# Kernel tuning notes

Measured on AMD Instinct MI355X. Metric: run time of the kernel, lower is better.

Reference implementation:

```python
import jax, jax.numpy as jnp
import numpy as np

B, N, E, ED, H, HID, OUT = 128, 100, 3200, 8, 4, 16, 32


def _ln(x, g, b):
    m = x.mean(-1, keepdims=True)
    v = ((x - m) ** 2).mean(-1, keepdims=True)
    return (x - m) / jnp.sqrt(v + 1e-5) * g + b


def _seg_softmax(logits, seg, n):
    # logits: [Etot, H], seg: [Etot] target node ids
    m = jax.ops.segment_max(logits, seg, num_segments=n)
    ex = jnp.exp(logits - m[seg])
    s = jax.ops.segment_sum(ex, seg, num_segments=n)
    return ex / (s[seg] + 1e-16)


def _tconv(x, src, dst, ea, Wq, bq, Wk, bk, Wv, bv, We, Ws, bs, heads, ch, n):
    # PyG TransformerConv, concat=False, root_weight=True, beta=False
    q = (x @ Wq.T + bq).reshape(-1, heads, ch)
    k = (x @ Wk.T + bk).reshape(-1, heads, ch)
    v = (x @ Wv.T + bv).reshape(-1, heads, ch)
    e = (ea @ We.T).reshape(-1, heads, ch)
    alpha = (q[dst] * (k[src] + e)).sum(-1) / jnp.sqrt(jnp.float32(ch))  # [Etot,H]
    alpha = _seg_softmax(alpha, dst, n)
    msg = (v[src] + e) * alpha[..., None]
    out = jax.ops.segment_sum(msg, dst, num_segments=n)  # [n,H,ch]
    out = out.mean(axis=1)  # concat=False -> head mean
    return out + x @ Ws.T + bs


def setup_inputs() -> dict:
    key = jax.random.key(0)
    ks = jax.random.split(key, 32)
    d = {}
    d['nodes_feats'] = jax.random.randint(ks[0], (B, N, 1), 0, 5).astype(jnp.float32)
    d['edge_index'] = jax.random.randint(ks[1], (B, 2, E), 0, N).astype(jnp.int32)
    d['edge_attr'] = jax.random.normal(ks[2], (B, E, ED), jnp.float32)
    d['agent_id'] = jax.random.randint(ks[3], (B, 1), 0, N).astype(jnp.int32)
    s = 0.1
    d['entity_embed'] = jax.random.normal(ks[4], (5, 4), jnp.float32)
    d['W1'] = jax.random.normal(ks[5], (HID, 4 + ED), jnp.float32) * s
    d['b1'] = jnp.zeros((HID,), jnp.float32)
    d['W2'] = jax.random.normal(ks[6], (HID, HID), jnp.float32) * s
    d['b2'] = jnp.zeros((HID,), jnp.float32)
    d['W3'] = jax.random.normal(ks[7], (HID, HID), jnp.float32) * s
    d['b3'] = jnp.zeros((HID,), jnp.float32)
    d['ln_g'] = jnp.ones((HID,), jnp.float32)
    d['ln_b'] = jnp.zeros((HID,), jnp.float32)
    i = 8
    for pre, ch, outd in (('g1', HID, HID), ('g2', OUT, OUT)):
        d[pre + '_Wq'] = jax.random.normal(ks[i + 0], (H * ch, HID), jnp.float32) * s
        d[pre + '_bq'] = jnp.zeros((H * ch,), jnp.float32)
        d[pre + '_Wk'] = jax.random.normal(ks[i + 1], (H * ch, HID), jnp.float32) * s
        d[pre + '_bk'] = jnp.zeros((H * ch,), jnp.float32)
        d[pre + '_Wv'] = jax.random.normal(ks[i + 2], (H * ch, HID), jnp.float32) * s
        d[pre + '_bv'] = jnp.zeros((H * ch,), jnp.float32)
        d[pre + '_We'] = jax.random.normal(ks[i + 3], (H * ch, ED), jnp.float32) * s
        d[pre + '_Ws'] = jax.random.normal(ks[i + 4], (outd, HID), jnp.float32) * s
        d[pre + '_bs'] = jnp.zeros((outd,), jnp.float32)
        i += 5
    return d


def reference(nodes_feats, edge_index, edge_attr, agent_id, entity_embed,
              W1, b1, W2, b2, W3, b3, ln_g, ln_b,
              g1_Wq, g1_bq, g1_Wk, g1_bk, g1_Wv, g1_bv, g1_We, g1_Ws, g1_bs,
              g2_Wq, g2_bq, g2_Wk, g2_bk, g2_Wv, g2_bv, g2_We, g2_Ws, g2_bs):
    n_tot = B * N
    # batched graph -> flat graph with per-batch node offsets
    offs = (jnp.arange(B, dtype=edge_index.dtype) * N)[:, None, None]
    ei = (edge_index + offs).transpose(1, 0, 2).reshape(2, -1)  # [2, B*E]
    src, dst = ei[0], ei[1]
    x = nodes_feats.reshape(-1, 1)            # [n_tot, 1]
    ea = edge_attr.reshape(-1, ED)            # [B*E, ED]

    # Embedding message-passing layer (aggr='add')
    etype = x[:, 0].astype(jnp.int32)[src]
    emb = entity_embed[etype]                  # [Etot, 4]
    h = jnp.concatenate([emb, ea], axis=1)
    h = _ln(jax.nn.relu(h @ W1.T + b1), ln_g, ln_b)
    h = _ln(jax.nn.relu(h @ W2.T + b2), ln_g, ln_b)
    h = _ln(jax.nn.relu(h @ W3.T + b3), ln_g, ln_b)
    z = jax.ops.segment_sum(h, dst, num_segments=n_tot)  # [n_tot, 16]

    a = _tconv(z, src, dst, ea, g1_Wq, g1_bq, g1_Wk, g1_bk, g1_Wv, g1_bv,
               g1_We, g1_Ws, g1_bs, H, HID, n_tot)
    a = _tconv(a, src, dst, ea, g2_Wq, g2_bq, g2_Wk, g2_bk, g2_Wv, g2_bv,
               g2_We, g2_Ws, g2_bs, H, OUT, n_tot)
    a = jax.nn.relu(a).reshape(B, N, OUT)
    # graph_aggr == 'agent': gather the agent node per batch
    out = jnp.take_along_axis(a, agent_id[:, :, None].astype(jnp.int32), axis=1)
    return out[:, 0, :]  # [B, OUT]
```

## Files before the change

kernel.cpp:

```cpp
#include <hip/hip_runtime.h>
#include <math.h>
#include <stdint.h>

#define Bb   128
#define Nn   100
#define Ee   3200
#define NTOT (Bb*Nn)
#define ETOT (Bb*Ee)



__global__ __launch_bounds__(1024) void k_csr(const int* __restrict__ ei,
                                              const int* __restrict__ agent,
                                              int* __restrict__ off,
                                              int2* __restrict__ cpair,
                                              int* __restrict__ mark)
{
    int b = ((blockIdx.x & 7) << 4) + (blockIdx.x >> 3);
    int t = threadIdx.x;
    __shared__ int s_src[Ee];
    __shared__ int s_dst[Ee];
    __shared__ int cnt[128];
    __shared__ int exc[128];
    __shared__ int cur[128];
    if (t < 128) cnt[t] = 0;
    if (t < Nn) mark[b * Nn + t] = 0;
    __syncthreads();
    const int* eis = ei + (size_t)b * 2 * Ee;
    const int* eid = eis + Ee;
    for (int e = t; e < Ee; e += 1024) {
        int s = eis[e];
        int d = eid[e];
        s_src[e] = s;
        s_dst[e] = d;
        atomicAdd(&cnt[d], 1);
    }
    __syncthreads();
    if (t < 64) {
        int c0 = cnt[2 * t];
        int c1 = cnt[2 * t + 1];
        int p = c0 + c1;
#pragma unroll
        for (int d = 1; d < 64; d <<= 1) {
            int v = __shfl_up(p, d);
            if (t >= d) p += v;
        }
        exc[2 * t]     = p - c0 - c1;
        exc[2 * t + 1] = p - c1;
        cur[2 * t]     = p - c0 - c1;
        cur[2 * t + 1] = p - c1;
    }
    __syncthreads();
    if (t < Nn) off[b * Nn + t] = b * Ee + exc[t];
    if (b == Bb - 1 && t == 0) off[NTOT] = ETOT;
    for (int e = t; e < Ee; e += 1024) {
        int d = s_dst[e];
        int idx = atomicAdd(&cur[d], 1);
        cpair[b * Ee + idx] = make_int2(s_src[e] + b * Nn, b * Ee + e);
    }
    int an = agent[b];
    if (t == 0) mark[b * Nn + an] = 1;
    for (int e = t; e < Ee; e += 1024) {
        if (s_dst[e] == an) mark[b * Nn + s_src[e]] = 1;
    }
}


__device__ __forceinline__ void ln_reg(float* h, const float* __restrict__ g,
                                       const float* __restrict__ b) {
    float s = 0.f;
#pragma unroll
    for (int c = 0; c < 16; c++) s += h[c];
    float m = s * 0.0625f;
    float v = 0.f;
#pragma unroll
    for (int c = 0; c < 16; c++) { float d = h[c] - m; v += d * d; }
    float r = rsqrtf(v * 0.0625f + 1e-5f);
#pragma unroll
    for (int c = 0; c < 16; c++) h[c] = (h[c] - m) * r * g[c] + b[c];
}

__global__ __launch_bounds__(256) void k_mlpz(
    const float* __restrict__ nf, const float* __restrict__ ea, const float* __restrict__ ee,
    const float* __restrict__ W1, const float* __restrict__ b1,
    const float* __restrict__ W2, const float* __restrict__ b2,
    const float* __restrict__ W3, const float* __restrict__ b3,
    const float* __restrict__ lg, const float* __restrict__ lb,
    const float* __restrict__ Wk, const float* __restrict__ bk,
    const float* __restrict__ Wv, const float* __restrict__ bv,
    const int* __restrict__ off, const int2* __restrict__ cpair,
    float* __restrict__ z, float* __restrict__ k1, float* __restrict__ v1)
{
    int lane = threadIdx.x & 63;
    int wid  = threadIdx.x >> 6;
    int n    = (blockIdx.x & 7) * (NTOT / 8) + (blockIdx.x >> 3) * 4 + wid;

    int o0 = off[n];
    int deg = off[n + 1] - o0;
    int chunks = (deg + 63) >> 6;

    float zs[16];
#pragma unroll
    for (int c = 0; c < 16; c++) zs[c] = 0.f;

    for (int ch = 0; ch < chunks; ch++) {
        int i = ch * 64 + lane;
        float h3[16];
        if (i < deg) {
            int2 p = cpair[o0 + i];
            int et = (int)nf[p.x];
            float in[12];
#pragma unroll
            for (int j = 0; j < 4; j++) in[j] = ee[et * 4 + j];
            const float4* ea4 = (const float4*)(ea + (size_t)p.y * 8);
            float4 ua = ea4[0], ub = ea4[1];
            in[4] = ua.x; in[5] = ua.y; in[6] = ua.z; in[7] = ua.w;
            in[8] = ub.x; in[9] = ub.y; in[10] = ub.z; in[11] = ub.w;

            float h1[16];
#pragma unroll
            for (int c = 0; c < 16; c++) {
                float s = b1[c];
#pragma unroll
                for (int j = 0; j < 12; j++) s = fmaf(W1[c * 12 + j], in[j], s);
                h1[c] = fmaxf(s, 0.f);
            }
            ln_reg(h1, lg, lb);
            float h2[16];
#pragma unroll
            for (int c = 0; c < 16; c++) {
                float s = b2[c];
#pragma unroll
                for (int j = 0; j < 16; j++) s = fmaf(W2[c * 16 + j], h1[j], s);
                h2[c] = fmaxf(s, 0.f);
            }
            ln_reg(h2, lg, lb);
#pragma unroll
            for (int c = 0; c < 16; c++) {
                float s = b3[c];
#pragma unroll
                for (int j = 0; j < 16; j++) s = fmaf(W3[c * 16 + j], h2[j], s);
                h3[c] = fmaxf(s, 0.f);
            }
            ln_reg(h3, lg, lb);
        } else {
#pragma unroll
            for (int c = 0; c < 16; c++) h3[c] = 0.f;
        }
#pragma unroll
        for (int c = 0; c < 16; c++) {
            float s = h3[c];
            s += __shfl_xor(s, 1);
            s += __shfl_xor(s, 2);
            s += __shfl_xor(s, 4);
            s += __shfl_xor(s, 8);
            s += __shfl_xor(s, 16);
            s += __shfl_xor(s, 32);
            zs[c] += s;
        }
    }

#pragma unroll
    for (int c = 0; c < 16; c++) if (lane == c) z[n * 16 + c] = zs[c];

    float ak = bk[lane], av = bv[lane];
#pragma unroll
    for (int j = 0; j < 16; j++) {
        ak = fmaf(Wk[lane * 16 + j], zs[j], ak);
        av = fmaf(Wv[lane * 16 + j], zs[j], av);
    }
    k1[n * 64 + lane] = ak;
    v1[n * 64 + lane] = av;
}


__global__ __launch_bounds__(256) void k_attn1(
    const float* __restrict__ ea,
    const float* __restrict__ k1, const float* __restrict__ v1,
    const float* __restrict__ z, const int* __restrict__ mark,
    const float* __restrict__ Wq, const float* __restrict__ bq,
    const float* __restrict__ We, const float* __restrict__ Ws, const float* __restrict__ bs,
    const int* __restrict__ off, const int2* __restrict__ cpair,
    float* __restrict__ a1)
{
    int n = (blockIdx.x & 7) * (NTOT / 8) + (blockIdx.x >> 3);
    if (!mark[n]) return;

    __shared__ float sm[4][64], sl[4][64], sa[4][64];
    int lane = threadIdx.x & 63;
    int w    = threadIdx.x >> 6;

    float zz[16];
#pragma unroll
    for (int j = 0; j < 16; j++) zz[j] = z[n * 16 + j];
    float ql = bq[lane];
#pragma unroll
    for (int j = 0; j < 16; j++) ql = fmaf(Wq[lane * 16 + j], zz[j], ql);
    float wer[8];
#pragma unroll
    for (int j = 0; j < 8; j++) wer[j] = We[lane * 8 + j];

    int o0  = off[n];
    int deg = off[n + 1] - o0;
    int i    = o0 + ((deg * w) >> 2);
    int iend = o0 + ((deg * (w + 1)) >> 2);

    float m = -1e30f, l = 0.f, acc = 0.f;
    for (; i + 2 <= iend; i += 2) {
        int2 pA = cpair[i];
        int2 pB = cpair[i + 1];
        const float4* eaA = (const float4*)(ea + (size_t)pA.y * 8);
        const float4* eaB = (const float4*)(ea + (size_t)pB.y * 8);
        float4 a0v = eaA[0], a1v = eaA[1], b0v = eaB[0], b1v = eaB[1];
        float eA = wer[0] * a0v.x + wer[1] * a0v.y + wer[2] * a0v.z + wer[3] * a0v.w
                 + wer[4] * a1v.x + wer[5] * a1v.y + wer[6] * a1v.z + wer[7] * a1v.w;
        float eB = wer[0] * b0v.x + wer[1] * b0v.y + wer[2] * b0v.z + wer[3] * b0v.w
                 + wer[4] * b1v.x + wer[5] * b1v.y + wer[6] * b1v.z + wer[7] * b1v.w;
        float kA = k1[(size_t)pA.x * 64 + lane];
        float kB = k1[(size_t)pB.x * 64 + lane];
        float vA = v1[(size_t)pA.x * 64 + lane];
        float vB = v1[(size_t)pB.x * 64 + lane];
        float tA = ql * (kA + eA);
        float tB = ql * (kB + eB);
        tA += __shfl_xor(tA, 1, 16);  tB += __shfl_xor(tB, 1, 16);
        tA += __shfl_xor(tA, 2, 16);  tB += __shfl_xor(tB, 2, 16);
        tA += __shfl_xor(tA, 4, 16);  tB += __shfl_xor(tB, 4, 16);
        tA += __shfl_xor(tA, 8, 16);  tB += __shfl_xor(tB, 8, 16);
        float lA  = tA * 0.25f;
        float lBv = tB * 0.25f;
        float nm = fmaxf(m, fmaxf(lA, lBv));
        float sc = __expf(m - nm);
        float wA = __expf(lA - nm);
        float wB = __expf(lBv - nm);
        acc = acc * sc + wA * (vA + eA) + wB * (vB + eB);
        l   = l * sc + wA + wB;
        m   = nm;
    }
    for (; i < iend; i++) {
        int2 p = cpair[i];
        const float4* ea4 = (const float4*)(ea + (size_t)p.y * 8);
        float4 u0 = ea4[0], u1 = ea4[1];
        float el = wer[0] * u0.x + wer[1] * u0.y + wer[2] * u0.z + wer[3] * u0.w
                 + wer[4] * u1.x + wer[5] * u1.y + wer[6] * u1.z + wer[7] * u1.w;
        float kl = k1[(size_t)p.x * 64 + lane];
        float tq = ql * (kl + el);
        tq += __shfl_xor(tq, 1, 16);
        tq += __shfl_xor(tq, 2, 16);
        tq += __shfl_xor(tq, 4, 16);
        tq += __shfl_xor(tq, 8, 16);
        float logit = tq * 0.25f;
        float nm = fmaxf(m, logit);
        float sc = __expf(m - nm);
        float wv = __expf(logit - nm);
        float vl = v1[(size_t)p.x * 64 + lane];
        acc = acc * sc + wv * (vl + el);
        l   = l * sc + wv;
        m   = nm;
    }
    sm[w][lane] = m; sl[w][lane] = l; sa[w][lane] = acc;
    __syncthreads();
    if (w == 0) {
        float M = fmaxf(fmaxf(sm[0][lane], sm[1][lane]), fmaxf(sm[2][lane], sm[3][lane]));
        float L = 0.f, A = 0.f;
#pragma unroll
        for (int ww = 0; ww < 4; ww++) {
            float sc = __expf(sm[ww][lane] - M);
            L += sc * sl[ww][lane];
            A += sc * sa[ww][lane];
        }
        float y = (deg > 0) ? (A / L) : 0.f;
        y += __shfl_xor(y, 16);
        y += __shfl_xor(y, 32);
        y *= 0.25f;
        if (lane < 16) {
            float r = bs[lane];
#pragma unroll
            for (int j = 0; j < 16; j++) r = fmaf(Ws[lane * 16 + j], zz[j], r);
            a1[n * 16 + lane] = y + r;
        }
    }
}


__global__ __launch_bounds__(512) void k_g2(
    const float* __restrict__ ea, const float* __restrict__ a1, const int* __restrict__ agent,
    const float* __restrict__ Wq, const float* __restrict__ bq,
    const float* __restrict__ Wk, const float* __restrict__ bk,
    const float* __restrict__ Wv, const float* __restrict__ bv,
    const float* __restrict__ We, const float* __restrict__ Ws, const float* __restrict__ bs,
    const int* __restrict__ off, const int2* __restrict__ cpair,
    float* __restrict__ out)
{
    __shared__ float sm[8][64], sl[8][64], sa0[8][64], sa1[8][64];
    int b = ((blockIdx.x & 7) << 4) + (blockIdx.x >> 3);
    int lane = threadIdx.x & 63;
    int w = threadIdx.x >> 6;
    int n = b * Nn + agent[b];
    int v0 = lane * 2, v1i = lane * 2 + 1;

    float aa[16];
#pragma unroll
    for (int j = 0; j < 16; j++) aa[j] = a1[n * 16 + j];

    float wk0[16], wk1[16], wv0[16], wv1[16], we0[8], we1[8];
#pragma unroll
    for (int j = 0; j < 16; j++) {
        wk0[j] = Wk[v0 * 16 + j];  wk1[j] = Wk[v1i * 16 + j];
        wv0[j] = Wv[v0 * 16 + j];  wv1[j] = Wv[v1i * 16 + j];
    }
#pragma unroll
    for (int j = 0; j < 8; j++) { we0[j] = We[v0 * 8 + j]; we1[j] = We[v1i * 8 + j]; }

    float q0 = bq[v0], q1v = bq[v1i];
#pragma unroll
    for (int j = 0; j < 16; j++) {
        q0  = fmaf(Wq[v0 * 16 + j],  aa[j], q0);
        q1v = fmaf(Wq[v1i * 16 + j], aa[j], q1v);
    }

    int o0 = off[n];
    int deg = off[n + 1] - o0;

    float m = -1e30f, l = 0.f, a0 = 0.f, a1c = 0.f;
    for (int i = w; i < deg; i += 8) {
        int2 p = cpair[o0 + i];
        int src = p.x, ge = p.y;
        float as[16];
#pragma unroll
        for (int j = 0; j < 16; j++) as[j] = a1[src * 16 + j];
        const float4* ea4 = (const float4*)(ea + (size_t)ge * 8);
        float4 u0 = ea4[0], u1 = ea4[1];
        float eav[8] = {u0.x, u0.y, u0.z, u0.w, u1.x, u1.y, u1.z, u1.w};

        float k0 = bk[v0], k1v = bk[v1i], vv0 = bv[v0], vv1 = bv[v1i];
#pragma unroll
        for (int j = 0; j < 16; j++) {
            k0  = fmaf(wk0[j], as[j], k0);
            k1v = fmaf(wk1[j], as[j], k1v);
            vv0 = fmaf(wv0[j], as[j], vv0);
            vv1 = fmaf(wv1[j], as[j], vv1);
        }
        float e0 = 0.f, e1 = 0.f;
#pragma unroll
        for (int j = 0; j < 8; j++) { e0 = fmaf(we0[j], eav[j], e0); e1 = fmaf(we1[j], eav[j], e1); }

        float t = q0 * (k0 + e0) + q1v * (k1v + e1);
        t += __shfl_xor(t, 1, 16);
        t += __shfl_xor(t, 2, 16);
        t += __shfl_xor(t, 4, 16);
        t += __shfl_xor(t, 8, 16);
        float logit = t * 0.17677669529663687f;
        float nm = fmaxf(m, logit);
        float sc = __expf(m - nm);
        float wgt = __expf(logit - nm);
        a0  = a0 * sc + wgt * (vv0 + e0);
        a1c = a1c * sc + wgt * (vv1 + e1);
        l   = l * sc + wgt;
        m   = nm;
    }
    sm[w][lane] = m; sl[w][lane] = l; sa0[w][lane] = a0; sa1[w][lane] = a1c;
    __syncthreads();
    if (w == 0) {
        float M = sm[0][lane];
#pragma unroll
        for (int ww = 1; ww < 8; ww++) M = fmaxf(M, sm[ww][lane]);
        float L = 0.f, A0 = 0.f, A1 = 0.f;
#pragma unroll
        for (int ww = 0; ww < 8; ww++) {
            float sc = __expf(sm[ww][lane] - M);
            L  += sc * sl[ww][lane];
            A0 += sc * sa0[ww][lane];
            A1 += sc * sa1[ww][lane];
        }
        float y0 = (deg > 0) ? (A0 / L) : 0.f;
        float y1 = (deg > 0) ? (A1 / L) : 0.f;
        y0 += __shfl_xor(y0, 16); y0 += __shfl_xor(y0, 32);
        y1 += __shfl_xor(y1, 16); y1 += __shfl_xor(y1, 32);
        y0 *= 0.25f; y1 *= 0.25f;

        if (lane < 16) {
            int c0 = lane * 2, c1 = lane * 2 + 1;
            float r0 = bs[c0], r1 = bs[c1];
#pragma unroll
            for (int j = 0; j < 16; j++) {
                r0 = fmaf(Ws[c0 * 16 + j], aa[j], r0);
                r1 = fmaf(Ws[c1 * 16 + j], aa[j], r1);
            }
            out[b * 32 + c0] = fmaxf(y0 + r0, 0.f);
            out[b * 32 + c1] = fmaxf(y1 + r1, 0.f);
        }
    }
}


extern "C" void kernel_launch(void* const* d_in, const int* in_sizes, int n_in,
                              void* d_out, int out_size, void* d_ws, size_t ws_size,
                              hipStream_t stream) {
    (void)in_sizes; (void)n_in; (void)out_size; (void)ws_size;
    const float* nf    = (const float*)d_in[0];
    const int*   ei    = (const int*)d_in[1];
    const float* ea    = (const float*)d_in[2];
    const int*   agent = (const int*)d_in[3];
    const float* ee    = (const float*)d_in[4];
    const float* W1    = (const float*)d_in[5];
    const float* b1    = (const float*)d_in[6];
    const float* W2    = (const float*)d_in[7];
    const float* b2    = (const float*)d_in[8];
    const float* W3    = (const float*)d_in[9];
    const float* b3    = (const float*)d_in[10];
    const float* lg    = (const float*)d_in[11];
    const float* lb    = (const float*)d_in[12];
    const float* g1Wq  = (const float*)d_in[13];
    const float* g1bq  = (const float*)d_in[14];
    const float* g1Wk  = (const float*)d_in[15];
    const float* g1bk  = (const float*)d_in[16];
    const float* g1Wv  = (const float*)d_in[17];
    const float* g1bv  = (const float*)d_in[18];
    const float* g1We  = (const float*)d_in[19];
    const float* g1Ws  = (const float*)d_in[20];
    const float* g1bs  = (const float*)d_in[21];
    const float* g2Wq  = (const float*)d_in[22];
    const float* g2bq  = (const float*)d_in[23];
    const float* g2Wk  = (const float*)d_in[24];
    const float* g2bk  = (const float*)d_in[25];
    const float* g2Wv  = (const float*)d_in[26];
    const float* g2bv  = (const float*)d_in[27];
    const float* g2We  = (const float*)d_in[28];
    const float* g2Ws  = (const float*)d_in[29];
    const float* g2bs  = (const float*)d_in[30];
    float* out = (float*)d_out;

    char* w = (char*)d_ws;
    int* mark  = (int*)w;  w += (size_t)NTOT * 4;
    int* off   = (int*)w;  w += (size_t)(NTOT + 4) * 4;
    w = (char*)(((uintptr_t)w + 15) & ~(uintptr_t)15);
    int2* cpair = (int2*)w; w += (size_t)ETOT * 8;
    float* z   = (float*)w; w += (size_t)NTOT * 16 * 4;
    float* k1  = (float*)w; w += (size_t)NTOT * 64 * 4;
    float* v1  = (float*)w; w += (size_t)NTOT * 64 * 4;
    float* a1  = (float*)w; w += (size_t)NTOT * 16 * 4;

    k_csr<<<dim3(Bb), dim3(1024), 0, stream>>>(ei, agent, off, cpair, mark);
    k_mlpz<<<dim3(NTOT / 4), dim3(256), 0, stream>>>(
        nf, ea, ee, W1, b1, W2, b2, W3, b3, lg, lb,
        g1Wk, g1bk, g1Wv, g1bv,
        off, cpair, z, k1, v1);
    k_attn1<<<dim3(NTOT), dim3(256), 0, stream>>>(
        ea, k1, v1, z, mark,
        g1Wq, g1bq, g1We, g1Ws, g1bs,
        off, cpair, a1);
    k_g2<<<dim3(Bb), dim3(512), 0, stream>>>(
        ea, a1, agent, g2Wq, g2bq, g2Wk, g2bk, g2Wv, g2bv, g2We, g2Ws, g2bs,
        off, cpair, out);
}
```

Baseline: 193.7 us.

## Fuse all four stages into one cooperative persistent kernel with grid syncs

```diff
diff --git a/kernel.cpp b/kernel.cpp
--- a/kernel.cpp
+++ b/kernel.cpp
@@ -1,6 +1,9 @@
 #include <hip/hip_runtime.h>
+#include <hip/hip_cooperative_groups.h>
 #include <math.h>
 #include <stdint.h>
+
+namespace cg = cooperative_groups;
 
 #define Bb   128
 #define Nn   100
@@ -8,6 +11,372 @@
 #define NTOT (Bb*Nn)
 #define ETOT (Bb*Ee)
 
+
+__device__ __forceinline__ void ln_reg(float* h, const float* __restrict__ g,
+                                       const float* __restrict__ b) {
+    float s = 0.f;
+#pragma unroll
+    for (int c = 0; c < 16; c++) s += h[c];
+    float m = s * 0.0625f;
+    float v = 0.f;
+#pragma unroll
+    for (int c = 0; c < 16; c++) { float d = h[c] - m; v += d * d; }
+    float r = rsqrtf(v * 0.0625f + 1e-5f);
+#pragma unroll
+    for (int c = 0; c < 16; c++) h[c] = (h[c] - m) * r * g[c] + b[c];
+}
+
+struct KParams {
+    const float *nf; const int *ei; const float *ea; const int *agent; const float *ee;
+    const float *W1, *b1, *W2, *b2, *W3, *b3, *lg, *lb;
+    const float *g1Wq, *g1bq, *g1Wk, *g1bk, *g1Wv, *g1bv, *g1We, *g1Ws, *g1bs;
+    const float *g2Wq, *g2bq, *g2Wk, *g2bk, *g2Wv, *g2bv, *g2We, *g2Ws, *g2bs;
+    float *out;
+    int *off; int2 *cpair; float *z, *k1, *v1, *a1; int *mlist, *mcnt;
+};
+
+
+__global__ __launch_bounds__(1024, 4) void k_all(KParams P)
+{
+    cg::grid_group grid = cg::this_grid();
+
+    __shared__ int s_src[Ee];
+    __shared__ int s_dst[Ee];
+    __shared__ int cnt[128], exc[128], cur[128];
+    __shared__ int smark[Nn], slist[Nn];
+    __shared__ int scnt;
+    __shared__ float dm[16][64], dl[16][64], d0[16][64], d1[16][64];
+
+    int t    = threadIdx.x;
+    int lane = t & 63;
+    int wid  = t >> 6;
+
+    if (blockIdx.x < 128) {
+        int b = ((blockIdx.x & 7) << 4) + (blockIdx.x >> 3);
+        if (t < 128) cnt[t] = 0;
+        if (t < Nn)  smark[t] = 0;
+        if (t == 0)  scnt = 0;
+        __syncthreads();
+        const int* eis = P.ei + (size_t)b * 2 * Ee;
+        const int* eid = eis + Ee;
+        for (int e = t; e < Ee; e += 1024) {
+            int s = eis[e];
+            int d = eid[e];
+            s_src[e] = s;
+            s_dst[e] = d;
+            atomicAdd(&cnt[d], 1);
+        }
+        __syncthreads();
+        if (t < 64) {
+            int c0 = cnt[2 * t];
+            int c1 = cnt[2 * t + 1];
+            int p = c0 + c1;
+#pragma unroll
+            for (int d = 1; d < 64; d <<= 1) {
+                int v = __shfl_up(p, d);
+                if (t >= d) p += v;
+            }
+            exc[2 * t]     = p - c0 - c1;
+            exc[2 * t + 1] = p - c1;
+            cur[2 * t]     = p - c0 - c1;
+            cur[2 * t + 1] = p - c1;
+        }
+        __syncthreads();
+        if (t < Nn) P.off[b * Nn + t] = b * Ee + exc[t];
+        if (b == Bb - 1 && t == 0) P.off[NTOT] = ETOT;
+        for (int e = t; e < Ee; e += 1024) {
+            int d = s_dst[e];
+            int idx = atomicAdd(&cur[d], 1);
+            P.cpair[b * Ee + idx] = make_int2(s_src[e] + b * Nn, b * Ee + e);
+        }
+        int an = P.agent[b];
+        if (t == 0) {
+            int old = atomicExch(&smark[an], 1);
+            if (!old) { int ix = atomicAdd(&scnt, 1); slist[ix] = an; }
+        }
+        for (int e = t; e < Ee; e += 1024) {
+            if (s_dst[e] == an) {
+                int s = s_src[e];
+                int old = atomicExch(&smark[s], 1);
+                if (!old) { int ix = atomicAdd(&scnt, 1); slist[ix] = s; }
+            }
+        }
+        __syncthreads();
+        if (t < scnt) P.mlist[b * Nn + t] = slist[t];
+        if (t == 0)   P.mcnt[b] = scnt;
+    }
+    grid.sync();
+
+    {
+        const int TW = 256 * 16;
+        for (int n = blockIdx.x * 16 + wid; n < NTOT; n += TW) {
+            int o0 = P.off[n];
+            int deg = P.off[n + 1] - o0;
+            int chunks = (deg + 63) >> 6;
+            float zs[16];
+#pragma unroll
+            for (int c = 0; c < 16; c++) zs[c] = 0.f;
+            for (int ch = 0; ch < chunks; ch++) {
+                int i = ch * 64 + lane;
+                float h3[16];
+                if (i < deg) {
+                    int2 p = P.cpair[o0 + i];
+                    int et = (int)P.nf[p.x];
+                    float in[12];
+#pragma unroll
+                    for (int j = 0; j < 4; j++) in[j] = P.ee[et * 4 + j];
+                    const float4* ea4 = (const float4*)(P.ea + (size_t)p.y * 8);
+                    float4 ua = ea4[0], ub = ea4[1];
+                    in[4] = ua.x; in[5] = ua.y; in[6] = ua.z; in[7] = ua.w;
+                    in[8] = ub.x; in[9] = ub.y; in[10] = ub.z; in[11] = ub.w;
+
+                    float h1[16];
+#pragma unroll
+                    for (int c = 0; c < 16; c++) {
+                        float s = P.b1[c];
+#pragma unroll
+                        for (int j = 0; j < 12; j++) s = fmaf(P.W1[c * 12 + j], in[j], s);
+                        h1[c] = fmaxf(s, 0.f);
+                    }
+                    ln_reg(h1, P.lg, P.lb);
+                    float h2[16];
+#pragma unroll
+                    for (int c = 0; c < 16; c++) {
+                        float s = P.b2[c];
+#pragma unroll
+                        for (int j = 0; j < 16; j++) s = fmaf(P.W2[c * 16 + j], h1[j], s);
+                        h2[c] = fmaxf(s, 0.f);
+                    }
+                    ln_reg(h2, P.lg, P.lb);
+#pragma unroll
+                    for (int c = 0; c < 16; c++) {
+                        float s = P.b3[c];
+#pragma unroll
+                        for (int j = 0; j < 16; j++) s = fmaf(P.W3[c * 16 + j], h2[j], s);
+                        h3[c] = fmaxf(s, 0.f);
+                    }
+                    ln_reg(h3, P.lg, P.lb);
+                } else {
+#pragma unroll
+                    for (int c = 0; c < 16; c++) h3[c] = 0.f;
+                }
+#pragma unroll
+                for (int c = 0; c < 16; c++) {
+                    float s = h3[c];
+                    s += __shfl_xor(s, 1);
+                    s += __shfl_xor(s, 2);
+                    s += __shfl_xor(s, 4);
+                    s += __shfl_xor(s, 8);
+                    s += __shfl_xor(s, 16);
+                    s += __shfl_xor(s, 32);
+                    zs[c] += s;
+                }
+            }
+#pragma unroll
+            for (int c = 0; c < 16; c++) if (lane == c) P.z[n * 16 + c] = zs[c];
+            float ak = P.g1bk[lane], av = P.g1bv[lane];
+#pragma unroll
+            for (int j = 0; j < 16; j++) {
+                ak = fmaf(P.g1Wk[lane * 16 + j], zs[j], ak);
+                av = fmaf(P.g1Wv[lane * 16 + j], zs[j], av);
+            }
+            P.k1[n * 64 + lane] = ak;
+            P.v1[n * 64 + lane] = av;
+        }
+    }
+    grid.sync();
+
+    {
+        int cb  = blockIdx.x;
+        int cl  = cb & 127;
+        int b   = ((cl & 7) << 4) + (cl >> 3);
+        int rep = cb >> 7;
+        int mc  = P.mcnt[b];
+        float wq[16], wer[8], ws1[16];
+#pragma unroll
+        for (int j = 0; j < 16; j++) wq[j] = P.g1Wq[lane * 16 + j];
+#pragma unroll
+        for (int j = 0; j < 8; j++) wer[j] = P.g1We[lane * 8 + j];
+        int lc = lane & 15;
+#pragma unroll
+        for (int j = 0; j < 16; j++) ws1[j] = P.g1Ws[lc * 16 + j];
+        float bq1 = P.g1bq[lane], bs1 = P.g1bs[lc];
+
+        for (int ix = rep * 16 + wid; ix < mc; ix += 32) {
+            int n = b * Nn + P.mlist[b * Nn + ix];
+            float zz[16];
+#pragma unroll
+            for (int j = 0; j < 16; j++) zz[j] = P.z[n * 16 + j];
+            float ql = bq1;
+#pragma unroll
+            for (int j = 0; j < 16; j++) ql = fmaf(wq[j], zz[j], ql);
+
+            int o0  = P.off[n];
+            int deg = P.off[n + 1] - o0;
+            int i = o0, iend = o0 + deg;
+
+            float m = -1e30f, l = 0.f, acc = 0.f;
+            for (; i + 2 <= iend; i += 2) {
+                int2 pA = P.cpair[i];
+                int2 pB = P.cpair[i + 1];
+                const float4* eaA = (const float4*)(P.ea + (size_t)pA.y * 8);
+                const float4* eaB = (const float4*)(P.ea + (size_t)pB.y * 8);
+                float4 a0v = eaA[0], a1v = eaA[1], b0v = eaB[0], b1v = eaB[1];
+                float eA = wer[0] * a0v.x + wer[1] * a0v.y + wer[2] * a0v.z + wer[3] * a0v.w
+                         + wer[4] * a1v.x + wer[5] * a1v.y + wer[6] * a1v.z + wer[7] * a1v.w;
+                float eB = wer[0] * b0v.x + wer[1] * b0v.y + wer[2] * b0v.z + wer[3] * b0v.w
+                         + wer[4] * b1v.x + wer[5] * b1v.y + wer[6] * b1v.z + wer[7] * b1v.w;
+                float kA = P.k1[(size_t)pA.x * 64 + lane];
+                float kB = P.k1[(size_t)pB.x * 64 + lane];
+                float vA = P.v1[(size_t)pA.x * 64 + lane];
+                float vB = P.v1[(size_t)pB.x * 64 + lane];
+                float tA = ql * (kA + eA);
+                float tB = ql * (kB + eB);
+                tA += __shfl_xor(tA, 1, 16);  tB += __shfl_xor(tB, 1, 16);
+                tA += __shfl_xor(tA, 2, 16);  tB += __shfl_xor(tB, 2, 16);
+                tA += __shfl_xor(tA, 4, 16);  tB += __shfl_xor(tB, 4, 16);
+                tA += __shfl_xor(tA, 8, 16);  tB += __shfl_xor(tB, 8, 16);
+                float lA  = tA * 0.25f;
+                float lBv = tB * 0.25f;
+                float nm = fmaxf(m, fmaxf(lA, lBv));
+                float sc = __expf(m - nm);
+                float wA = __expf(lA - nm);
+                float wB = __expf(lBv - nm);
+                acc = acc * sc + wA * (vA + eA) + wB * (vB + eB);
+                l   = l * sc + wA + wB;
+                m   = nm;
+            }
+            for (; i < iend; i++) {
+                int2 p = P.cpair[i];
+                const float4* ea4 = (const float4*)(P.ea + (size_t)p.y * 8);
+                float4 u0 = ea4[0], u1 = ea4[1];
+                float el = wer[0] * u0.x + wer[1] * u0.y + wer[2] * u0.z + wer[3] * u0.w
+                         + wer[4] * u1.x + wer[5] * u1.y + wer[6] * u1.z + wer[7] * u1.w;
+                float kl = P.k1[(size_t)p.x * 64 + lane];
+                float tq = ql * (kl + el);
+                tq += __shfl_xor(tq, 1, 16);
+                tq += __shfl_xor(tq, 2, 16);
+                tq += __shfl_xor(tq, 4, 16);
+                tq += __shfl_xor(tq, 8, 16);
+                float logit = tq * 0.25f;
+                float nm = fmaxf(m, logit);
+                float sc = __expf(m - nm);
+                float wv = __expf(logit - nm);
+                float vl = P.v1[(size_t)p.x * 64 + lane];
+                acc = acc * sc + wv * (vl + el);
+                l   = l * sc + wv;
+                m   = nm;
+            }
+            float y = (deg > 0) ? (acc / l) : 0.f;
+            y += __shfl_xor(y, 16);
+            y += __shfl_xor(y, 32);
+            y *= 0.25f;
+            float r = bs1;
+#pragma unroll
+            for (int j = 0; j < 16; j++) r = fmaf(ws1[j], zz[j], r);
+            if (lane < 16) P.a1[n * 16 + lane] = y + r;
+        }
+    }
+    grid.sync();
+
+    if (blockIdx.x < 128) {
+        int b = ((blockIdx.x & 7) << 4) + (blockIdx.x >> 3);
+        int n = b * Nn + P.agent[b];
+        int v0 = lane * 2, v1i = lane * 2 + 1;
+
+        float aa[16];
+#pragma unroll
+        for (int j = 0; j < 16; j++) aa[j] = P.a1[n * 16 + j];
+
+        float wk0[16], wk1[16], wv0[16], wv1[16], we0[8], we1[8];
+#pragma unroll
+        for (int j = 0; j < 16; j++) {
+            wk0[j] = P.g2Wk[v0 * 16 + j];  wk1[j] = P.g2Wk[v1i * 16 + j];
+            wv0[j] = P.g2Wv[v0 * 16 + j];  wv1[j] = P.g2Wv[v1i * 16 + j];
+        }
+#pragma unroll
+        for (int j = 0; j < 8; j++) { we0[j] = P.g2We[v0 * 8 + j]; we1[j] = P.g2We[v1i * 8 + j]; }
+
+        float q0 = P.g2bq[v0], q1v = P.g2bq[v1i];
+#pragma unroll
+        for (int j = 0; j < 16; j++) {
+            q0  = fmaf(P.g2Wq[v0 * 16 + j],  aa[j], q0);
+            q1v = fmaf(P.g2Wq[v1i * 16 + j], aa[j], q1v);
+        }
+
+        int o0 = P.off[n];
+        int deg = P.off[n + 1] - o0;
+
+        float m = -1e30f, l = 0.f, a0 = 0.f, a1c = 0.f;
+        for (int i = wid; i < deg; i += 16) {
+            int2 p = P.cpair[o0 + i];
+            float as[16];
+#pragma unroll
+            for (int j = 0; j < 16; j++) as[j] = P.a1[(size_t)p.x * 16 + j];
+            const float4* ea4 = (const float4*)(P.ea + (size_t)p.y * 8);
+            float4 u0 = ea4[0], u1 = ea4[1];
+            float eav[8] = {u0.x, u0.y, u0.z, u0.w, u1.x, u1.y, u1.z, u1.w};
+
+            float k0 = P.g2bk[v0], k1v = P.g2bk[v1i], vv0 = P.g2bv[v0], vv1 = P.g2bv[v1i];
+#pragma unroll
+            for (int j = 0; j < 16; j++) {
+                k0  = fmaf(wk0[j], as[j], k0);
+                k1v = fmaf(wk1[j], as[j], k1v);
+                vv0 = fmaf(wv0[j], as[j], vv0);
+                vv1 = fmaf(wv1[j], as[j], vv1);
+            }
+            float e0 = 0.f, e1 = 0.f;
+#pragma unroll
+            for (int j = 0; j < 8; j++) { e0 = fmaf(we0[j], eav[j], e0); e1 = fmaf(we1[j], eav[j], e1); }
+
+            float tq = q0 * (k0 + e0) + q1v * (k1v + e1);
+            tq += __shfl_xor(tq, 1, 16);
+            tq += __shfl_xor(tq, 2, 16);
+            tq += __shfl_xor(tq, 4, 16);
+            tq += __shfl_xor(tq, 8, 16);
+            float logit = tq * 0.17677669529663687f;
+            float nm = fmaxf(m, logit);
+            float sc = __expf(m - nm);
+            float wgt = __expf(logit - nm);
+            a0  = a0 * sc + wgt * (vv0 + e0);
+            a1c = a1c * sc + wgt * (vv1 + e1);
+            l   = l * sc + wgt;
+            m   = nm;
+        }
+        dm[wid][lane] = m; dl[wid][lane] = l; d0[wid][lane] = a0; d1[wid][lane] = a1c;
+        __syncthreads();
+        if (wid == 0) {
+            float M = dm[0][lane];
+#pragma unroll
+            for (int ww = 1; ww < 16; ww++) M = fmaxf(M, dm[ww][lane]);
+            float L = 0.f, A0 = 0.f, A1 = 0.f;
+#pragma unroll
+            for (int ww = 0; ww < 16; ww++) {
+                float sc = __expf(dm[ww][lane] - M);
+                L  += sc * dl[ww][lane];
+                A0 += sc * d0[ww][lane];
+                A1 += sc * d1[ww][lane];
+            }
+            float y0 = (deg > 0) ? (A0 / L) : 0.f;
+            float y1 = (deg > 0) ? (A1 / L) : 0.f;
+            y0 += __shfl_xor(y0, 16); y0 += __shfl_xor(y0, 32);
+            y1 += __shfl_xor(y1, 16); y1 += __shfl_xor(y1, 32);
+            y0 *= 0.25f; y1 *= 0.25f;
+
+            if (lane < 16) {
+                int c0 = lane * 2, c1 = lane * 2 + 1;
+                float r0 = P.g2bs[c0], r1 = P.g2bs[c1];
+#pragma unroll
+                for (int j = 0; j < 16; j++) {
+                    r0 = fmaf(P.g2Ws[c0 * 16 + j], aa[j], r0);
+                    r1 = fmaf(P.g2Ws[c1 * 16 + j], aa[j], r1);
+                }
+                P.out[b * 32 + c0] = fmaxf(y0 + r0, 0.f);
+                P.out[b * 32 + c1] = fmaxf(y1 + r1, 0.f);
+            }
+        }
+    }
+}
 
 
 __global__ __launch_bounds__(1024) void k_csr(const int* __restrict__ ei,
@@ -65,21 +434,6 @@
     }
 }
 
-
-__device__ __forceinline__ void ln_reg(float* h, const float* __restrict__ g,
-                                       const float* __restrict__ b) {
-    float s = 0.f;
-#pragma unroll
-    for (int c = 0; c < 16; c++) s += h[c];
-    float m = s * 0.0625f;
-    float v = 0.f;
-#pragma unroll
-    for (int c = 0; c < 16; c++) { float d = h[c] - m; v += d * d; }
-    float r = rsqrtf(v * 0.0625f + 1e-5f);
-#pragma unroll
-    for (int c = 0; c < 16; c++) h[c] = (h[c] - m) * r * g[c] + b[c];
-}
-
 __global__ __launch_bounds__(256) void k_mlpz(
     const float* __restrict__ nf, const float* __restrict__ ea, const float* __restrict__ ee,
     const float* __restrict__ W1, const float* __restrict__ b1,
@@ -172,7 +526,6 @@
     k1[n * 64 + lane] = ak;
     v1[n * 64 + lane] = av;
 }
-
 
 __global__ __launch_bounds__(256) void k_attn1(
     const float* __restrict__ ea,
@@ -281,7 +634,6 @@
     }
 }
 
-
 __global__ __launch_bounds__(512) void k_g2(
     const float* __restrict__ ea, const float* __restrict__ a1, const int* __restrict__ agent,
     const float* __restrict__ Wq, const float* __restrict__ bq,
@@ -324,11 +676,10 @@
     float m = -1e30f, l = 0.f, a0 = 0.f, a1c = 0.f;
     for (int i = w; i < deg; i += 8) {
         int2 p = cpair[o0 + i];
-        int src = p.x, ge = p.y;
         float as[16];
 #pragma unroll
-        for (int j = 0; j < 16; j++) as[j] = a1[src * 16 + j];
-        const float4* ea4 = (const float4*)(ea + (size_t)ge * 8);
+        for (int j = 0; j < 16; j++) as[j] = a1[(size_t)p.x * 16 + j];
+        const float4* ea4 = (const float4*)(ea + (size_t)p.y * 8);
         float4 u0 = ea4[0], u1 = ea4[1];
         float eav[8] = {u0.x, u0.y, u0.z, u0.w, u1.x, u1.y, u1.z, u1.w};
 
@@ -431,7 +782,6 @@
     float* out = (float*)d_out;
 
     char* w = (char*)d_ws;
-    int* mark  = (int*)w;  w += (size_t)NTOT * 4;
     int* off   = (int*)w;  w += (size_t)(NTOT + 4) * 4;
     w = (char*)(((uintptr_t)w + 15) & ~(uintptr_t)15);
     int2* cpair = (int2*)w; w += (size_t)ETOT * 8;
@@ -439,17 +789,37 @@
     float* k1  = (float*)w; w += (size_t)NTOT * 64 * 4;
     float* v1  = (float*)w; w += (size_t)NTOT * 64 * 4;
     float* a1  = (float*)w; w += (size_t)NTOT * 16 * 4;
-
-    k_csr<<<dim3(Bb), dim3(1024), 0, stream>>>(ei, agent, off, cpair, mark);
-    k_mlpz<<<dim3(NTOT / 4), dim3(256), 0, stream>>>(
-        nf, ea, ee, W1, b1, W2, b2, W3, b3, lg, lb,
-        g1Wk, g1bk, g1Wv, g1bv,
-        off, cpair, z, k1, v1);
-    k_attn1<<<dim3(NTOT), dim3(256), 0, stream>>>(
-        ea, k1, v1, z, mark,
-        g1Wq, g1bq, g1We, g1Ws, g1bs,
-        off, cpair, a1);
-    k_g2<<<dim3(Bb), dim3(512), 0, stream>>>(
-        ea, a1, agent, g2Wq, g2bq, g2Wk, g2bk, g2Wv, g2bv, g2We, g2Ws, g2bs,
-        off, cpair, out);
+    int* mark  = (int*)w;  w += (size_t)NTOT * 4;
+    int* mlist = (int*)w;  w += (size_t)NTOT * 4;
+    int* mcnt  = (int*)w;  w += (size_t)Bb * 4;
+
+    KParams P;
+    P.nf = nf; P.ei = ei; P.ea = ea; P.agent = agent; P.ee = ee;
+    P.W1 = W1; P.b1 = b1; P.W2 = W2; P.b2 = b2; P.W3 = W3; P.b3 = b3;
+    P.lg = lg; P.lb = lb;
+    P.g1Wq = g1Wq; P.g1bq = g1bq; P.g1Wk = g1Wk; P.g1bk = g1bk;
+    P.g1Wv = g1Wv; P.g1bv = g1bv; P.g1We = g1We; P.g1Ws = g1Ws; P.g1bs = g1bs;
+    P.g2Wq = g2Wq; P.g2bq = g2bq; P.g2Wk = g2Wk; P.g2bk = g2bk;
+    P.g2Wv = g2Wv; P.g2bv = g2bv; P.g2We = g2We; P.g2Ws = g2Ws; P.g2bs = g2bs;
+    P.out = out;
+    P.off = off; P.cpair = cpair; P.z = z; P.k1 = k1; P.v1 = v1; P.a1 = a1;
+    P.mlist = mlist; P.mcnt = mcnt;
+
+    void* kargs[] = { (void*)&P };
+    hipError_t err = hipLaunchCooperativeKernel((const void*)k_all, dim3(256), dim3(1024),
+                                                kargs, 0, stream);
+    if (err != hipSuccess) {
+        k_csr<<<dim3(Bb), dim3(1024), 0, stream>>>(ei, agent, off, cpair, mark);
+        k_mlpz<<<dim3(NTOT / 4), dim3(256), 0, stream>>>(
+            nf, ea, ee, W1, b1, W2, b2, W3, b3, lg, lb,
+            g1Wk, g1bk, g1Wv, g1bv,
+            off, cpair, z, k1, v1);
+        k_attn1<<<dim3(NTOT), dim3(256), 0, stream>>>(
+            ea, k1, v1, z, mark,
+            g1Wq, g1bq, g1We, g1Ws, g1bs,
+            off, cpair, a1);
+        k_g2<<<dim3(Bb), dim3(512), 0, stream>>>(
+            ea, a1, agent, g2Wq, g2bq, g2Wk, g2bk, g2Wv, g2bv, g2We, g2Ws, g2bs,
+            off, cpair, out);
+    }
 }
```

Measured after the change: 464.6 us. +139.9%, slower.
